# Optimization experiments

Measured on AMD Instinct MI355X. Metric: run time of the kernel, lower is better.

Reference implementation:

```python
import jax, jax.numpy as jnp
import numpy as np

SIZE, D, N, E = 50000, 1024, 50000, 100000


def setup_inputs() -> dict:
    key = jax.random.key(0)
    k1, k2 = jax.random.split(key)
    # torchhd.embeddings.Random produces bipolar {-1,+1} MAP hypervectors
    w = jnp.where(jax.random.uniform(k1, (SIZE, D)) < 0.5, -1.0, 1.0).astype(jnp.float32)
    edge_index = jax.random.randint(k2, (2, E), 0, N, dtype=jnp.int32)
    return {"node_ids_weight": w, "edge_index": edge_index, "num_nodes": N}


def reference(node_ids_weight, edge_index, num_nodes):
    # degree_centrality: in-degree via bincount on columns, normalized
    col = edge_index[1]
    degree = jnp.bincount(col, length=num_nodes)
    pr = degree / num_nodes  # float
    pr_argsort = jnp.argsort(pr)  # stable sort, matches torch sort semantics on ties

    # node_id_hvs[pr_argsort] = weight[:num_nodes]  (scatter assign)
    node_id_hvs = jnp.zeros((num_nodes, node_ids_weight.shape[1]),
                            dtype=node_ids_weight.dtype)
    node_id_hvs = node_id_hvs.at[pr_argsort].set(node_ids_weight[:num_nodes])

    # to_undirected: sort endpoints per edge, then unique columns.
    # jit-friendly unique: lexsort edges, mask out duplicates of the previous edge.
    e = jnp.sort(edge_index, axis=0)  # [2, E], row <= col per edge
    order = jnp.lexsort((e[1], e[0]))
    r = e[0][order]
    c = e[1][order]
    keep = jnp.concatenate([
        jnp.array([True]),
        (r[1:] != r[:-1]) | (c[1:] != c[:-1]),
    ])  # [E] True for first occurrence of each unique edge

    # bind = elementwise multiply of gathered hvs; multiset = sum over edges
    hvs = node_id_hvs[r] * node_id_hvs[c]  # [E, D]
    out = jnp.sum(jnp.where(keep[:, None], hvs, 0.0), axis=0)  # [D]
    return out
```

## Files before the change

### kernel.cpp

```cpp
#include <hip/hip_runtime.h>
#include <stdint.h>

#define DCAP   128
#define CHUNK  1024
#define LOG_TAB 19
#define TAB_SIZE (1u << LOG_TAB)
#define TAB_MASK (TAB_SIZE - 1u)
#define KEMPTY 0xFFFFFFFFu

__global__ void k_degree(const int* __restrict__ col, int* __restrict__ degree, int E) {
    int e = blockIdx.x * blockDim.x + threadIdx.x;
    if (e < E) atomicAdd(&degree[col[e]], 1);
}

__global__ void k_chunk_hist(const int* __restrict__ degree, int* __restrict__ hist,
                             int* __restrict__ chunkHist, int N) {
    __shared__ int sh[DCAP];
    int t = threadIdx.x;
    if (t < DCAP) sh[t] = 0;
    __syncthreads();
    int j = blockIdx.x * CHUNK + t;
    if (j < N) {
        int d = degree[j];
        if (d < DCAP) atomicAdd(&sh[d], 1);
        else          atomicAdd(&hist[d], 1);
    }
    __syncthreads();
    if (t < DCAP) chunkHist[blockIdx.x * DCAP + t] = sh[t];
}

__global__ void k_chunk_prefix(int* __restrict__ hist, int* __restrict__ chunkHist,
                               int numChunks) {
    __shared__ int stot[DCAP];
    int d = threadIdx.x;
    int tot = 0;
    for (int c = 0; c < numChunks; ++c) tot += chunkHist[c * DCAP + d];
    stot[d] = tot;
    hist[d] = tot;
    __syncthreads();
    int run = 0;
    for (int d2 = 0; d2 < d; ++d2) run += stot[d2];
    for (int c = 0; c < numChunks; ++c) {
        int tmp = chunkHist[c * DCAP + d];
        chunkHist[c * DCAP + d] = run;
        run += tmp;
    }
}

__global__ void k_pos_small(const int* __restrict__ degree, const int* __restrict__ chunkBase,
                            int* __restrict__ pos, int N) {
    __shared__ int sdeg[CHUNK];
    int t = threadIdx.x;
    int j = blockIdx.x * CHUNK + t;
    int d = (j < N) ? degree[j] : -1;
    sdeg[t] = d;
    __syncthreads();
    if (j < N && d < DCAP) {
        int r = 0;
        for (int t2 = 0; t2 < t; ++t2) r += (sdeg[t2] == d);
        pos[j] = chunkBase[blockIdx.x * DCAP + d] + r;
    }
}

__global__ void k_pos_large(const int* __restrict__ degree, const int* __restrict__ hist,
                            int* __restrict__ pos, int N, int E) {
    int d = DCAP + blockIdx.x * blockDim.x + threadIdx.x;
    if (d > E) return;
    if (hist[d] == 0) return;
    int base = 0;
    for (int d2 = 0; d2 < d; ++d2) base += hist[d2];
    int cnt = 0;
    for (int j = 0; j < N; ++j)
        if (degree[j] == d) pos[j] = base + cnt++;
}

__global__ __launch_bounds__(256) void k_pack_ballot(const float* __restrict__ W,
                                                     uint32_t* __restrict__ Wbits) {
    long long idx = (long long)blockIdx.x * 256 + threadIdx.x;
    const uint4 u = ((const uint4*)W)[idx];
    int lane = threadIdx.x & 63;
    unsigned long long m0 = __ballot((int)u.x < 0);
    unsigned long long m1 = __ballot((int)u.y < 0);
    unsigned long long m2 = __ballot((int)u.z < 0);
    unsigned long long m3 = __ballot((int)u.w < 0);
    if (lane < 8) {
        int k = lane >> 1, half = lane & 1;
        unsigned long long m = (k == 0) ? m0 : (k == 1) ? m1 : (k == 2) ? m2 : m3;
        uint32_t w32 = half ? (uint32_t)(m >> 32) : (uint32_t)m;
        long long gwave = idx >> 6;
        Wbits[gwave * 8 + lane] = w32;
    }
}

__global__ __launch_bounds__(256) void k_pack_linear(const float* __restrict__ W,
                                                     uint32_t* __restrict__ Wbits, long long NW) {
    long long widx = (long long)blockIdx.x * 256 + threadIdx.x;
    if (widx >= NW) return;
    const uint4* src = (const uint4*)(W + widx * 32);
    uint32_t word = 0;
    #pragma unroll
    for (int q = 0; q < 8; ++q) {
        uint4 u = src[q];
        word |= (u.x >> 31) << (4 * q + 0);
        word |= (u.y >> 31) << (4 * q + 1);
        word |= (u.z >> 31) << (4 * q + 2);
        word |= (u.w >> 31) << (4 * q + 3);
    }
    Wbits[widx] = word;
}

__global__ void k_insert(const int* __restrict__ ei, const int* __restrict__ pos,
                         unsigned int* __restrict__ tab, int* __restrict__ uA,
                         int* __restrict__ uB, int* __restrict__ count, int E) {
    int e = blockIdx.x * blockDim.x + threadIdx.x;
    if (e >= E) return;
    int a = ei[e], b = ei[E + e];
    int r = min(a, b), c = max(a, b);
    unsigned int key = ((unsigned int)r << 16) | (unsigned int)c;
    unsigned int h = (key * 2654435761u) >> (32 - LOG_TAB);
    while (true) {
        unsigned int old = atomicCAS(&tab[h], KEMPTY, key);
        if (old == KEMPTY) {
            int idx = atomicAdd(count, 1);
            uA[idx] = pos[r];
            uB[idx] = pos[c];
            return;
        }
        if (old == key) return;
        h = (h + 1) & TAB_MASK;
    }
}

__global__ __launch_bounds__(256) void k_accum_bits(const uint32_t* __restrict__ Wbits,
                                                    const int* __restrict__ uA,
                                                    const int* __restrict__ uB,
                                                    const int* __restrict__ count,
                                                    int* __restrict__ neg, int D) {
    __shared__ int sneg[1024];
    int t = threadIdx.x;
    int w = t & 31;
    int slot = t >> 5;
    int wpr = D / 32;
    for (int i = t; i < D; i += 256) sneg[i] = 0;
    __syncthreads();
    int cnt = *count;
    int cnts[32];
    #pragma unroll
    for (int d = 0; d < 32; ++d) cnts[d] = 0;
    for (int base = blockIdx.x * 8; base < cnt; base += gridDim.x * 8) {
        int e = base + slot;
        if (e < cnt) {
            uint32_t a = Wbits[(size_t)uA[e] * wpr + w];
            uint32_t b = Wbits[(size_t)uB[e] * wpr + w];
            uint32_t x = a ^ b;
            #pragma unroll
            for (int d = 0; d < 32; ++d) cnts[d] += (x >> d) & 1u;
        }
    }
    #pragma unroll
    for (int d = 0; d < 32; ++d) atomicAdd(&sneg[w * 32 + d], cnts[d]);
    __syncthreads();
    for (int i = t; i < D; i += 256)
        if (sneg[i]) atomicAdd(&neg[i], sneg[i]);
}

__global__ void k_finalize(const int* __restrict__ neg, const int* __restrict__ count,
                           float* __restrict__ out, int D, int permuted) {
    int d = blockIdx.x * blockDim.x + threadIdx.x;
    if (d >= D) return;
    int ni;
    if (permuted) {
        int off = d & 255, q = d >> 8;
        int k = off & 3, l = off >> 2, half = l >> 5, b = l & 31;
        ni = (q * 8 + 2 * k + half) * 32 + b;
    } else {
        ni = d;
    }
    out[d] = (float)(*count - 2 * neg[ni]);
}

static inline size_t align256(size_t x) { return (x + 255) & ~(size_t)255; }

extern "C" void kernel_launch(void* const* d_in, const int* in_sizes, int n_in,
                              void* d_out, int out_size, void* d_ws, size_t ws_size,
                              hipStream_t stream) {
    const float* W  = (const float*)d_in[0];
    const int*   ei = (const int*)d_in[1];
    const int D = out_size;
    const int N = in_sizes[0] / D;
    const int E = in_sizes[1] / 2;
    const int numChunks = (N + CHUNK - 1) / CHUNK;
    const long long ND = (long long)N * D;
    const long long NW = ND / 32;

    char* p = (char*)d_ws;
    char* zbase = p;
    int* degree       = (int*)p;          p += align256((size_t)N * 4);
    int* hist         = (int*)p;          p += align256((size_t)(E + 1) * 4);
    int* count        = (int*)p;          p += 256;
    int* neg          = (int*)p;          p += align256((size_t)D * 4);
    size_t zbytes = (size_t)(p - zbase);
    int* chunkHist    = (int*)p;          p += align256((size_t)numChunks * DCAP * 4);
    int* pos          = (int*)p;          p += align256((size_t)N * 4);
    unsigned int* tab = (unsigned int*)p; p += (size_t)TAB_SIZE * 4;
    int* uA           = (int*)p;          p += align256((size_t)E * 4);
    int* uB           = (int*)p;          p += align256((size_t)E * 4);
    uint32_t* Wbits   = (uint32_t*)p;     p += align256((size_t)NW * 4);

    hipMemsetAsync(zbase, 0, zbytes, stream);
    hipMemsetAsync(tab, 0xFF, (size_t)TAB_SIZE * 4, stream);

    k_degree<<<(E + 255) / 256, 256, 0, stream>>>(ei + E, degree, E);
    k_chunk_hist<<<numChunks, CHUNK, 0, stream>>>(degree, hist, chunkHist, N);
    k_chunk_prefix<<<1, DCAP, 0, stream>>>(hist, chunkHist, numChunks);
    k_pos_small<<<numChunks, CHUNK, 0, stream>>>(degree, chunkHist, pos, N);
    int nLarge = E + 1 - DCAP;
    k_pos_large<<<(nLarge + 255) / 256, 256, 0, stream>>>(degree, hist, pos, N, E);

    int permuted = (D % 256 == 0) && (ND % 1024 == 0);
    if (permuted) {
        k_pack_ballot<<<(int)(ND / 1024), 256, 0, stream>>>(W, Wbits);
    } else {
        k_pack_linear<<<(int)((NW + 255) / 256), 256, 0, stream>>>(W, Wbits, NW);
    }

    k_insert<<<(E + 255) / 256, 256, 0, stream>>>(ei, pos, tab, uA, uB, count, E);
    k_accum_bits<<<1024, 256, 0, stream>>>(Wbits, uA, uB, count, neg, D);
    k_finalize<<<(D + 255) / 256, 256, 0, stream>>>(neg, count, (float*)d_out, D, permuted);
}
```

Baseline: 140.0 us.

## Fuse memsets into one init kernel, grid-stride pack, smaller histogram chunks

```diff
diff --git a/kernel.cpp b/kernel.cpp
--- a/kernel.cpp
+++ b/kernel.cpp
@@ -2,11 +2,21 @@
 #include <stdint.h>
 
 #define DCAP   128
-#define CHUNK  1024
+#define CHUNK  256
 #define LOG_TAB 19
 #define TAB_SIZE (1u << LOG_TAB)
 #define TAB_MASK (TAB_SIZE - 1u)
 #define KEMPTY 0xFFFFFFFFu
+
+__global__ __launch_bounds__(256) void k_init(uint4* __restrict__ z, int zn4,
+                                              uint4* __restrict__ t, int tn4) {
+    int stride = gridDim.x * 256;
+    int i = blockIdx.x * 256 + threadIdx.x;
+    uint4 zero = make_uint4(0u, 0u, 0u, 0u);
+    uint4 ones = make_uint4(~0u, ~0u, ~0u, ~0u);
+    for (int j = i; j < zn4; j += stride) z[j] = zero;
+    for (int j = i; j < tn4; j += stride) t[j] = ones;
+}
 
 __global__ void k_degree(const int* __restrict__ col, int* __restrict__ degree, int E) {
     int e = blockIdx.x * blockDim.x + threadIdx.x;
@@ -75,20 +85,30 @@
 }
 
 __global__ __launch_bounds__(256) void k_pack_ballot(const float* __restrict__ W,
-                                                     uint32_t* __restrict__ Wbits) {
-    long long idx = (long long)blockIdx.x * 256 + threadIdx.x;
-    const uint4 u = ((const uint4*)W)[idx];
+                                                     uint32_t* __restrict__ Wbits,
+                                                     long long G) {
+    long long wv0 = ((long long)blockIdx.x * 256 + threadIdx.x) >> 6;
+    long long nwv = ((long long)gridDim.x * 256) >> 6;
     int lane = threadIdx.x & 63;
-    unsigned long long m0 = __ballot((int)u.x < 0);
-    unsigned long long m1 = __ballot((int)u.y < 0);
-    unsigned long long m2 = __ballot((int)u.z < 0);
-    unsigned long long m3 = __ballot((int)u.w < 0);
-    if (lane < 8) {
-        int k = lane >> 1, half = lane & 1;
-        unsigned long long m = (k == 0) ? m0 : (k == 1) ? m1 : (k == 2) ? m2 : m3;
-        uint32_t w32 = half ? (uint32_t)(m >> 32) : (uint32_t)m;
-        long long gwave = idx >> 6;
-        Wbits[gwave * 8 + lane] = w32;
+    int k = lane >> 1, half = lane & 1;
+    const uint4* W4 = (const uint4*)W;
+    for (long long gb = wv0 * 4; gb < G; gb += nwv * 4) {
+        #pragma unroll
+        for (int s = 0; s < 4; ++s) {
+            long long g = gb + s;
+            if (g < G) {
+                uint4 u = W4[g * 64 + lane];
+                unsigned long long m0 = __ballot((int)u.x < 0);
+                unsigned long long m1 = __ballot((int)u.y < 0);
+                unsigned long long m2 = __ballot((int)u.z < 0);
+                unsigned long long m3 = __ballot((int)u.w < 0);
+                if (lane < 8) {
+                    unsigned long long m = (k == 0) ? m0 : (k == 1) ? m1
+                                         : (k == 2) ? m2 : m3;
+                    Wbits[g * 8 + lane] = half ? (uint32_t)(m >> 32) : (uint32_t)m;
+                }
+            }
+        }
     }
 }
 
@@ -207,8 +227,10 @@
     int* uB           = (int*)p;          p += align256((size_t)E * 4);
     uint32_t* Wbits   = (uint32_t*)p;     p += align256((size_t)NW * 4);
 
-    hipMemsetAsync(zbase, 0, zbytes, stream);
-    hipMemsetAsync(tab, 0xFF, (size_t)TAB_SIZE * 4, stream);
+    int zn4 = (int)(zbytes / 16);
+    int tn4 = (int)((size_t)TAB_SIZE * 4 / 16);
+    int initGrid = (max(zn4, tn4) + 255) / 256;
+    k_init<<<initGrid, 256, 0, stream>>>((uint4*)zbase, zn4, (uint4*)tab, tn4);
 
     k_degree<<<(E + 255) / 256, 256, 0, stream>>>(ei + E, degree, E);
     k_chunk_hist<<<numChunks, CHUNK, 0, stream>>>(degree, hist, chunkHist, N);
@@ -217,9 +239,10 @@
     int nLarge = E + 1 - DCAP;
     k_pos_large<<<(nLarge + 255) / 256, 256, 0, stream>>>(degree, hist, pos, N, E);
 
-    int permuted = (D % 256 == 0) && (ND % 1024 == 0);
+    int permuted = (D % 256 == 0);
     if (permuted) {
-        k_pack_ballot<<<(int)(ND / 1024), 256, 0, stream>>>(W, Wbits);
+        long long G = ND / 256;
+        k_pack_ballot<<<2048, 256, 0, stream>>>(W, Wbits, G);
     } else {
         k_pack_linear<<<(int)((NW + 255) / 256), 256, 0, stream>>>(W, Wbits, NW);
     }
```

Result: slower. 160.3 us (+14.5%).
